# Kernel tuning notes

Hardware: AMD Instinct MI355X
Metric: run time of the kernel (lower is better)

## Reference

```python
import jax, jax.numpy as jnp
import numpy as np

B, T, N_EMBD, H = 8, 2048, 1024, 128

def setup_inputs() -> dict:
    key = jax.random.key(0)
    k1, k2, k3, k4 = jax.random.split(key, 4)
    x = jax.random.normal(k1, (B, T, N_EMBD), dtype=jnp.float32)
    s = 1.0 / np.sqrt(N_EMBD).astype(np.float32)
    Wq = jax.random.normal(k2, (N_EMBD, H), dtype=jnp.float32) * s
    Wk = jax.random.normal(k3, (N_EMBD, H), dtype=jnp.float32) * s
    Wv = jax.random.normal(k4, (N_EMBD, H), dtype=jnp.float32) * s
    return {"x": x, "Wq": Wq, "Wk": Wk, "Wv": Wv}

def reference(x, Wq, Wk, Wv):
    # x: [B,T,C]; projections (no bias per init_kwargs)
    q = x @ Wq  # [B,T,H]
    k = x @ Wk  # [B,T,H]
    v = x @ Wv  # [B,T,H]
    scale = jnp.asarray(k.shape[-1], x.dtype) ** -0.5
    att = jnp.einsum('bth,bsh->bts', q, k) * scale  # [B,T,T]
    Tlen = x.shape[1]
    causal = jnp.tril(jnp.ones((Tlen, Tlen), dtype=bool))  # bias buffer tril mask
    att = jnp.where(causal, att, jnp.asarray(-jnp.inf, att.dtype))
    att = jax.nn.softmax(att, axis=-1)
    # dropout omitted (eval mode / deterministic reference)
    y = jnp.einsum('bts,bsh->bth', att, v)  # [B,T,H]
    return y
```

## Files before the change

kernel.cpp:

```cpp
#include <hip/hip_runtime.h>
#include <hip/hip_bf16.h>
#include <stdint.h>

#define BB 8
#define TT 2048
#define CC 1024
#define HH 128
#define VTP 2112

typedef __attribute__((ext_vector_type(8))) short bf16x8;
typedef __attribute__((ext_vector_type(8))) unsigned short u16x8;
typedef __attribute__((ext_vector_type(4))) float f32x4;
typedef __attribute__((ext_vector_type(8))) _Float16 h16x8;

static __device__ __forceinline__ unsigned short f2bf(float f) {
    union { float f; uint32_t u; } v; v.f = f;
    return (unsigned short)((v.u + 0x7fffu + ((v.u >> 16) & 1u)) >> 16);
}

#define GLOBAL_AS __attribute__((address_space(1)))
#define LDS_AS    __attribute__((address_space(3)))
static __device__ __forceinline__ void async16(const void* g, void* l) {
    __builtin_amdgcn_global_load_lds((const GLOBAL_AS void*)g, (LDS_AS void*)l, 16, 0, 0);
}

__global__ __launch_bounds__(256) void wconv(
    const float* __restrict__ Wq, const float* __restrict__ Wk,
    const float* __restrict__ Wv, unsigned short* __restrict__ Wb)
{
    int u = blockIdx.x * 256 + threadIdx.x;
    if (u >= 3 * 128 * 128) return;
    int kc = u & 127, n = (u >> 7) & 127, mat = u >> 14;
    const float* W = (mat == 0) ? Wq : (mat == 1) ? Wk : Wv;
    const float* s = W + (size_t)(kc * 8) * HH + n;
    u16x8 v;
    #pragma unroll
    for (int j = 0; j < 8; j++) v[j] = f2bf(s[(size_t)j * HH]);
    *(u16x8*)(Wb + ((size_t)mat * HH + n) * CC + kc * 8) = v;
}

#define BS_U16 4608
#define EQ_OFF 0
#define EK_OFF 8704
#define EV_OFF 17408
__global__ __launch_bounds__(512) void qkv_proj(
    const float* __restrict__ x, const unsigned short* __restrict__ Wb,
    unsigned short* __restrict__ Q, unsigned short* __restrict__ K,
    unsigned short* __restrict__ Vt)
{
    __shared__ __align__(16) unsigned short lds[29184];

    const int m0  = blockIdx.x * 64;
    const int tid = threadIdx.x;
    const int lane = tid & 63;
    const int w    = tid >> 6;
    const int qd   = lane >> 4;
    const int ln   = lane & 15;
    const int wm   = w & 1;
    const int wn   = w >> 1;

    f32x4 acc[2][6];
    #pragma unroll
    for (int i = 0; i < 2; i++)
        #pragma unroll
        for (int j = 0; j < 6; j++) acc[i][j] = (f32x4){0.f,0.f,0.f,0.f};

    const int xr = tid >> 3;
    const int xg = (tid & 7) * 8;

    float4 xf[2];
    {
        const float* s = x + (size_t)(m0 + xr) * CC + xg;
        xf[0] = ((const float4*)s)[0];
        xf[1] = ((const float4*)s)[1];
    }

    for (int k0 = 0; k0 < CC; k0 += 64) {
        {
            u16x8 v0;
            v0[0]=f2bf(xf[0].x); v0[1]=f2bf(xf[0].y); v0[2]=f2bf(xf[0].z); v0[3]=f2bf(xf[0].w);
            v0[4]=f2bf(xf[1].x); v0[5]=f2bf(xf[1].y); v0[6]=f2bf(xf[1].z); v0[7]=f2bf(xf[1].w);
            *(u16x8*)&lds[xr * 72 + xg] = v0;
        }
        #pragma unroll
        for (int i = 0; i < 6; i++) {
            int sb = i * 512 + w * 64;
            int slot = sb + lane;
            int row = slot >> 3, j = (slot & 7) ^ (row & 7);
            async16(Wb + (size_t)row * CC + k0 + j * 8, &lds[BS_U16 + sb * 8]);
        }
        __syncthreads();
        if (k0 + 64 < CC) {
            const float* s = x + (size_t)(m0 + xr) * CC + k0 + 64 + xg;
            xf[0] = ((const float4*)s)[0];
            xf[1] = ((const float4*)s)[1];
        }
        #pragma unroll
        for (int ks = 0; ks < 2; ks++) {
            bf16x8 a0 = *(const bf16x8*)&lds[(wm*32 + ln) * 72 + ks*32 + qd*8];
            bf16x8 a1 = *(const bf16x8*)&lds[(wm*32 + 16 + ln) * 72 + ks*32 + qd*8];
            #pragma unroll
            for (int nf = 0; nf < 6; nf++) {
                int row = wn * 96 + nf * 16 + ln;
                int ch  = (ks * 4 + qd) ^ (row & 7);
                bf16x8 b = *(const bf16x8*)&lds[BS_U16 + (row * 8 + ch) * 8];
                acc[0][nf] = __builtin_amdgcn_mfma_f32_16x16x32_bf16(a0, b, acc[0][nf], 0, 0, 0);
                acc[1][nf] = __builtin_amdgcn_mfma_f32_16x16x32_bf16(a1, b, acc[1][nf], 0, 0, 0);
            }
        }
        __syncthreads();
    }

    #pragma unroll
    for (int mf = 0; mf < 2; mf++)
        #pragma unroll
        for (int nf = 0; nf < 6; nf++) {
            int n = wn * 96 + nf * 16;
            int mat = n >> 7, hb = n & 127;
            #pragma unroll
            for (int r = 0; r < 4; r++) {
                unsigned short v = f2bf(acc[mf][nf][r]);
                int mrow = wm*32 + mf*16 + qd*4 + r;
                if (mat < 2) lds[(mat ? EK_OFF : EQ_OFF) + mrow * 136 + hb + ln] = v;
                else         lds[EV_OFF + (hb + ln) * 72 + mrow] = v;
            }
        }
    __syncthreads();
    {
        int rr = tid >> 3, c0 = (tid & 7) * 16;
        #pragma unroll
        for (int i = 0; i < 2; i++) {
            u16x8 vq = *(const u16x8*)&lds[EQ_OFF + rr * 136 + c0 + i * 8];
            *(u16x8*)(Q + (size_t)(m0 + rr) * HH + c0 + i * 8) = vq;
            u16x8 vk = *(const u16x8*)&lds[EK_OFF + rr * 136 + c0 + i * 8];
            *(u16x8*)(K + (size_t)(m0 + rr) * HH + c0 + i * 8) = vk;
        }
    }
    {
        int bb = m0 >> 11, t0 = m0 & (TT - 1);
        int hh = tid >> 2, tf = (tid & 3) * 16;
        #pragma unroll
        for (int i = 0; i < 2; i++) {
            u16x8 vv = *(const u16x8*)&lds[EV_OFF + hh * 72 + tf + i * 8];
            *(u16x8*)(Vt + ((size_t)bb * HH + hh) * VTP + t0 + tf + i * 8) = vv;
        }
    }
}

__global__ __launch_bounds__(512) void attn(
    const unsigned short* __restrict__ Q, const unsigned short* __restrict__ K,
    const unsigned short* __restrict__ Vt, float* __restrict__ out)
{
    __shared__ __align__(16) unsigned short Ks[128 * 128];
    __shared__ __align__(16) unsigned short Vs[128 * 128];
    __shared__ __align__(16) unsigned short Ps[8][16 * 40];
    __shared__ float Lp[8][16];

    const int tid  = threadIdx.x;
    const int lane = tid & 63;
    const int wave = tid >> 6;
    const int qd = lane >> 4;
    const int ln = lane & 15;
    const int qgrp = wave >> 2;
    const int kq4  = wave & 3;

    const int bx = blockIdx.x;
    int b, qt;
    if (bx < 256) { b = bx & 7;               qt = 63 - (bx >> 3); }
    else          { int u = bx - 256; b = u & 7; qt = u >> 3; }
    const int qbase = qt * 32 + qgrp * 16;
    const int nst = (qt + 4) >> 2;

    const unsigned short* Qb = Q  + (size_t)b * TT * HH;
    const unsigned short* Kb = K  + (size_t)b * TT * HH;
    const unsigned short* Vb = Vt + (size_t)b * HH * VTP;

    bf16x8 aq[4];
    #pragma unroll
    for (int c = 0; c < 4; c++)
        aq[c] = *(const bf16x8*)(Qb + (size_t)(qbase + ln) * HH + c * 32 + qd * 8);

    f32x4 O[8];
    float lsum[4];
    #pragma unroll
    for (int h = 0; h < 8; h++) O[h] = (f32x4){0.f,0.f,0.f,0.f};
    #pragma unroll
    for (int r = 0; r < 4; r++) lsum[r] = 0.f;

    const float sl   = 0.08838834764831843f * 1.4426950408889634f;
    const float M0L2 = 7.2134752044448f;
    unsigned short* ps = Ps[wave];

    for (int st = 0; st < nst; st++) {
        const int s0 = st * 128;
        #pragma unroll
        for (int i = 0; i < 4; i++) {
            int sb = i * 512 + wave * 64;
            int slot = sb + lane;
            int row = slot >> 4, jj = (slot & 15) ^ (row & 15);
            async16(Kb + (size_t)(s0 + row) * HH + jj * 8, &Ks[sb * 8]);
        }
        #pragma unroll
        for (int i = 0; i < 4; i++) {
            int sb = i * 512 + wave * 64;
            int slot = sb + lane;
            int row = slot >> 4, jj = (slot & 15) ^ (row & 15);
            async16(Vb + (size_t)row * VTP + s0 + jj * 8, &Vs[sb * 8]);
        }
        __syncthreads();

        f32x4 s[2] = {(f32x4){0.f,0.f,0.f,0.f}, (f32x4){0.f,0.f,0.f,0.f}};
        #pragma unroll
        for (int nt = 0; nt < 2; nt++) {
            int krow = kq4 * 32 + nt * 16;
            #pragma unroll
            for (int c = 0; c < 4; c++) {
                bf16x8 bk = *(const bf16x8*)&Ks[(krow + ln) * 128 + (((c*4 + qd) ^ ln)) * 8];
                s[nt] = __builtin_amdgcn_mfma_f32_16x16x32_bf16(aq[c], bk, s[nt], 0, 0, 0);
            }
        }
        #pragma unroll
        for (int nt = 0; nt < 2; nt++) {
            int col = s0 + kq4 * 32 + nt * 16 + ln;
            #pragma unroll
            for (int r = 0; r < 4; r++) {
                int row = qbase + qd * 4 + r;
                float e = __builtin_amdgcn_exp2f(s[nt][r] * sl - M0L2);
                e = (col <= row) ? e : 0.f;
                lsum[r] += e;
                ps[(qd*4 + r) * 40 + nt*16 + ln] = f2bf(e);
            }
        }
        bf16x8 ap = *(const bf16x8*)&ps[ln * 40 + qd * 8];
        #pragma unroll
        for (int ht = 0; ht < 8; ht++) {
            int vrow = ht * 16 + ln;
            bf16x8 bv = *(const bf16x8*)&Vs[vrow * 128 + (((kq4*4 + qd) ^ ln)) * 8];
            O[ht] = __builtin_amdgcn_mfma_f32_16x16x32_bf16(ap, bv, O[ht], 0, 0, 0);
        }
        if (st + 1 < nst) __syncthreads();
    }

    __syncthreads();
    #pragma unroll
    for (int r = 0; r < 4; r++) {
        float sum = lsum[r];
        #pragma unroll
        for (int off = 1; off < 16; off <<= 1)
            sum += __shfl_xor(sum, off, 64);
        if (ln == 0) Lp[wave][qd*4 + r] = sum;
    }
    _Float16* om = (_Float16*)&Ks[0] + (size_t)wave * 16 * 128;
    #pragma unroll
    for (int ht = 0; ht < 8; ht++)
        #pragma unroll
        for (int r = 0; r < 4; r++)
            om[(qd*4 + r) * 128 + ht*16 + ln] = (_Float16)O[ht][r];
    __syncthreads();

    {
        int row = tid >> 4, h0 = (tid & 15) * 8;
        int g = row >> 4, q = row & 15;
        float L = Lp[g*4 + 0][q] + Lp[g*4 + 1][q] + Lp[g*4 + 2][q] + Lp[g*4 + 3][q];
        float inv = 1.0f / L;
        const _Float16* p0 = (const _Float16*)&Ks[0] + (size_t)(g*4 + 0) * 2048 + q * 128 + h0;
        const _Float16* p1 = p0 + 2048;
        const _Float16* p2 = p1 + 2048;
        const _Float16* p3 = p2 + 2048;
        float* op = out + ((size_t)b * TT + qt * 32 + row) * HH + h0;
        #pragma unroll
        for (int i = 0; i < 2; i++) {
            float4 v;
            v.x = (((float)p0[i*4+0] + (float)p1[i*4+0]) + ((float)p2[i*4+0] + (float)p3[i*4+0])) * inv;
            v.y = (((float)p0[i*4+1] + (float)p1[i*4+1]) + ((float)p2[i*4+1] + (float)p3[i*4+1])) * inv;
            v.z = (((float)p0[i*4+2] + (float)p1[i*4+2]) + ((float)p2[i*4+2] + (float)p3[i*4+2])) * inv;
            v.w = (((float)p0[i*4+3] + (float)p1[i*4+3]) + ((float)p2[i*4+3] + (float)p3[i*4+3])) * inv;
            ((float4*)op)[i] = v;
        }
    }
}

extern "C" void kernel_launch(void* const* d_in, const int* in_sizes, int n_in,
                              void* d_out, int out_size, void* d_ws, size_t ws_size,
                              hipStream_t stream) {
    const float* x  = (const float*)d_in[0];
    const float* Wq = (const float*)d_in[1];
    const float* Wk = (const float*)d_in[2];
    const float* Wv = (const float*)d_in[3];

    unsigned short* Wb = (unsigned short*)d_ws;
    unsigned short* Qw = Wb + (size_t)3 * HH * CC;
    unsigned short* Kw = Qw + (size_t)BB * TT * HH;
    unsigned short* Vw = Kw + (size_t)BB * TT * HH;

    wconv<<<dim3(192), 256, 0, stream>>>(Wq, Wk, Wv, Wb);
    qkv_proj<<<dim3(256), 512, 0, stream>>>(x, Wb, Qw, Kw, Vw);
    attn<<<dim3(512), 512, 0, stream>>>(Qw, Kw, Vw, (float*)d_out);
}
```

Baseline: 149.2 us.

## Load K and V tiles directly from global memory instead of staging in LDS

Removes the async global-to-LDS staging of the K and V tiles and the per-iteration block barriers. Each wave now reads its MFMA operands for K and transposed V straight from global memory, relying on L1/L2 for reuse. LDS use drops to a dedicated output-reduction buffer, which may raise occupancy. In exchange, the two query groups that share each K/V slice now load it separately from global memory, and the loads are no longer prefetched in bulk, so memory latency may be exposed on the MFMA path.

```diff
diff --git a/kernel.cpp b/kernel.cpp
--- a/kernel.cpp
+++ b/kernel.cpp
@@ -151,8 +151,7 @@
     const unsigned short* __restrict__ Q, const unsigned short* __restrict__ K,
     const unsigned short* __restrict__ Vt, float* __restrict__ out)
 {
-    __shared__ __align__(16) unsigned short Ks[128 * 128];
-    __shared__ __align__(16) unsigned short Vs[128 * 128];
+    __shared__ __align__(16) _Float16 Om[8][16 * 128];
     __shared__ __align__(16) unsigned short Ps[8][16 * 40];
     __shared__ float Lp[8][16];
 
@@ -193,29 +192,14 @@
 
     for (int st = 0; st < nst; st++) {
         const int s0 = st * 128;
-        #pragma unroll
-        for (int i = 0; i < 4; i++) {
-            int sb = i * 512 + wave * 64;
-            int slot = sb + lane;
-            int row = slot >> 4, jj = (slot & 15) ^ (row & 15);
-            async16(Kb + (size_t)(s0 + row) * HH + jj * 8, &Ks[sb * 8]);
-        }
-        #pragma unroll
-        for (int i = 0; i < 4; i++) {
-            int sb = i * 512 + wave * 64;
-            int slot = sb + lane;
-            int row = slot >> 4, jj = (slot & 15) ^ (row & 15);
-            async16(Vb + (size_t)row * VTP + s0 + jj * 8, &Vs[sb * 8]);
-        }
-        __syncthreads();
 
         f32x4 s[2] = {(f32x4){0.f,0.f,0.f,0.f}, (f32x4){0.f,0.f,0.f,0.f}};
         #pragma unroll
         for (int nt = 0; nt < 2; nt++) {
-            int krow = kq4 * 32 + nt * 16;
+            const unsigned short* kr = Kb + (size_t)(s0 + kq4*32 + nt*16 + ln) * HH;
             #pragma unroll
             for (int c = 0; c < 4; c++) {
-                bf16x8 bk = *(const bf16x8*)&Ks[(krow + ln) * 128 + (((c*4 + qd) ^ ln)) * 8];
+                bf16x8 bk = *(const bf16x8*)(kr + (c*4 + qd) * 8);
                 s[nt] = __builtin_amdgcn_mfma_f32_16x16x32_bf16(aq[c], bk, s[nt], 0, 0, 0);
             }
         }
@@ -234,14 +218,11 @@
         bf16x8 ap = *(const bf16x8*)&ps[ln * 40 + qd * 8];
         #pragma unroll
         for (int ht = 0; ht < 8; ht++) {
-            int vrow = ht * 16 + ln;
-            bf16x8 bv = *(const bf16x8*)&Vs[vrow * 128 + (((kq4*4 + qd) ^ ln)) * 8];
+            bf16x8 bv = *(const bf16x8*)(Vb + (size_t)(ht*16 + ln) * VTP + s0 + kq4*32 + qd*8);
             O[ht] = __builtin_amdgcn_mfma_f32_16x16x32_bf16(ap, bv, O[ht], 0, 0, 0);
         }
-        if (st + 1 < nst) __syncthreads();
-    }
-
-    __syncthreads();
+    }
+
     #pragma unroll
     for (int r = 0; r < 4; r++) {
         float sum = lsum[r];
@@ -250,7 +231,7 @@
             sum += __shfl_xor(sum, off, 64);
         if (ln == 0) Lp[wave][qd*4 + r] = sum;
     }
-    _Float16* om = (_Float16*)&Ks[0] + (size_t)wave * 16 * 128;
+    _Float16* om = &Om[wave][0];
     #pragma unroll
     for (int ht = 0; ht < 8; ht++)
         #pragma unroll
@@ -263,10 +244,10 @@
         int g = row >> 4, q = row & 15;
         float L = Lp[g*4 + 0][q] + Lp[g*4 + 1][q] + Lp[g*4 + 2][q] + Lp[g*4 + 3][q];
         float inv = 1.0f / L;
-        const _Float16* p0 = (const _Float16*)&Ks[0] + (size_t)(g*4 + 0) * 2048 + q * 128 + h0;
-        const _Float16* p1 = p0 + 2048;
-        const _Float16* p2 = p1 + 2048;
-        const _Float16* p3 = p2 + 2048;
+        const _Float16* p0 = &Om[g*4 + 0][q * 128 + h0];
+        const _Float16* p1 = &Om[g*4 + 1][q * 128 + h0];
+        const _Float16* p2 = &Om[g*4 + 2][q * 128 + h0];
+        const _Float16* p3 = &Om[g*4 + 3][q * 128 + h0];
         float* op = out + ((size_t)b * TT + qt * 32 + row) * HH + h0;
         #pragma unroll
         for (int i = 0; i < 2; i++) {
```

New measurement: 180.3 us. 20.9% more time.
